# Performance work log

Measured on AMD Instinct MI355X. Metric: run time of the kernel, lower is better.

## Reference

```python
import jax, jax.numpy as jnp
import numpy as np

EPS = 0.0  # module eps default
N, C = 524288, 128


def setup_inputs() -> dict:
    key = jax.random.key(0)
    x = jax.random.normal(key, (N, C), dtype=jnp.float32)
    return {"x": x}


def reference(x):
    n, c = x.shape
    # mean over batch (H=W=1 in the original NCHW view)
    m = jnp.mean(x, axis=0, keepdims=True)          # [1, C]
    xn = x - m                                      # [N, C]
    # covariance: T @ T.T / (N-1) with T = xn.T -> [C, C]
    f_cov = jnp.einsum('ni,nj->ij', xn, xn) / (n - 1)
    eye = jnp.eye(c, dtype=x.dtype)
    f_cov_shrinked = (1.0 - EPS) * f_cov + EPS * eye
    L = jnp.linalg.cholesky(f_cov_shrinked)         # lower-triangular
    # inv_sqrt = L^{-1} via triangular solve of L @ X = I
    inv_sqrt = jax.scipy.linalg.solve_triangular(L, eye, lower=True)  # [C, C]
    # 1x1 conv with kernel inv_sqrt[o, i] == xn @ inv_sqrt.T
    decorrelated = xn @ inv_sqrt.T                  # [N, C]
    return decorrelated
```

## Files before the change

### kernel.cpp

```cpp
#include <hip/hip_runtime.h>

#define NROWS 524288
#define NCH 128
#define GSTR 40

typedef __attribute__((ext_vector_type(8))) short bf16x8;
typedef __attribute__((ext_vector_type(4))) float f32x4;

#define BARRIER_ND() asm volatile("s_waitcnt lgkmcnt(0)\ns_barrier" ::: "memory")

static __device__ __forceinline__ unsigned short f2bf_rne(float f) {
    unsigned u = __float_as_uint(f);
    return (unsigned short)((u + 0x7FFFu + ((u >> 16) & 1u)) >> 16);
}

static __device__ __forceinline__ bf16x8 ldfrag(const unsigned short* base, int c, int s0) {
    int m = (c >> 3) & 12;
    return *(const bf16x8*)(base + c * GSTR + 2 * (s0 ^ m));
}

#define PACKW1(B, c, x0, x1, csacc) do {                                      \
    unsigned u0 = __float_as_uint(x0), u1 = __float_as_uint(x1);              \
    unsigned packH = (u0 >> 16) | (u1 & 0xFFFF0000u);                         \
    float l0_ = 2.0f * ((x0) - __uint_as_float(u0 & 0xFFFF0000u));            \
    float l1_ = 2.0f * ((x1) - __uint_as_float(u1 & 0xFFFF0000u));            \
    unsigned packL = (unsigned)f2bf_rne(l0_) | ((unsigned)f2bf_rne(l1_) << 16); \
    int idx_ = (c) * GSTR + 2 * (p ^ (cg & 12));                              \
    *(unsigned*)&XT[B][0][idx_] = packH;                                      \
    *(unsigned*)&XT[B][1][idx_] = packL;                                      \
    csacc += (x0) + (x1);                                                     \
} while (0)

#define LOADR(ci, r0, r1, r2, r3) do {                                        \
    const float4* s4_ = (const float4*)x + ((size_t)(ci) * 32 + 2 * p) * 32 + cg * 2; \
    r0 = s4_[0]; r1 = s4_[1]; r2 = s4_[32]; r3 = s4_[33];                     \
} while (0)

#define PACKALL(B, r0, r1, r2, r3) do {                                       \
    PACKW1(B, cg * 8 + 0, r0.x, r2.x, cs0);                                   \
    PACKW1(B, cg * 8 + 1, r0.y, r2.y, cs1);                                   \
    PACKW1(B, cg * 8 + 2, r0.z, r2.z, cs2);                                   \
    PACKW1(B, cg * 8 + 3, r0.w, r2.w, cs3);                                   \
    PACKW1(B, cg * 8 + 4, r1.x, r3.x, cs4);                                   \
    PACKW1(B, cg * 8 + 5, r1.y, r3.y, cs5);                                   \
    PACKW1(B, cg * 8 + 6, r1.z, r3.z, cs6);                                   \
    PACKW1(B, cg * 8 + 7, r1.w, r3.w, cs7);                                   \
} while (0)

#define MFMA_STEP(B) do {                                                     \
    const unsigned short* Xh = &XT[B][0][0];                                  \
    const unsigned short* Xl = &XT[B][1][0];                                  \
    bf16x8 ah0 = ldfrag(Xh, (2 * w + 0) * 16 + lc, ls);                       \
    bf16x8 ah1 = ldfrag(Xh, (2 * w + 1) * 16 + lc, ls);                       \
    _Pragma("unroll")                                                         \
    for (int tj = 0; tj < 8; ++tj) {                                          \
        bf16x8 bh = ldfrag(Xh, tj * 16 + lc, ls);                             \
        bf16x8 bl = ldfrag(Xl, tj * 16 + lc, ls);                             \
        acc[0][tj] = __builtin_amdgcn_mfma_f32_16x16x32_bf16(ah0, bh, acc[0][tj], 0, 0, 0); \
        acc[0][tj] = __builtin_amdgcn_mfma_f32_16x16x32_bf16(ah0, bl, acc[0][tj], 0, 0, 0); \
        acc[1][tj] = __builtin_amdgcn_mfma_f32_16x16x32_bf16(ah1, bh, acc[1][tj], 0, 0, 0); \
        acc[1][tj] = __builtin_amdgcn_mfma_f32_16x16x32_bf16(ah1, bl, acc[1][tj], 0, 0, 0); \
    }                                                                         \
} while (0)

template <int STORE>
__global__ __launch_bounds__(256, 4) void k_gram(const float* __restrict__ x,
                                                 float* __restrict__ part,
                                                 float* __restrict__ colpart,
                                                 float* __restrict__ gram,
                                                 float* __restrict__ colsum,
                                                 int cpb) {
    __shared__ __align__(16) unsigned short XT[2][2][128 * GSTR];
    const int tid = threadIdx.x;
    const int w = tid >> 6;
    const int l = tid & 63;
    const int lc = l & 15;
    const int ls = (l >> 4) * 4;
    const int p = tid >> 4;
    const int cg = tid & 15;

    f32x4 acc[2][8];
#pragma unroll
    for (int a = 0; a < 2; ++a)
#pragma unroll
        for (int t = 0; t < 8; ++t) acc[a][t] = (f32x4){0.f, 0.f, 0.f, 0.f};
    float cs0 = 0.f, cs1 = 0.f, cs2 = 0.f, cs3 = 0.f;
    float cs4 = 0.f, cs5 = 0.f, cs6 = 0.f, cs7 = 0.f;

    const int c0 = blockIdx.x * cpb;
    float4 a0, a1, a2, a3, b0, b1, b2, b3;

    LOADR(c0 + 0, a0, a1, a2, a3);
    LOADR(c0 + 1, b0, b1, b2, b3);
    PACKALL(0, a0, a1, a2, a3);
    BARRIER_ND();

#pragma unroll 1
    for (int t = 0; t < cpb; t += 2) {
        MFMA_STEP(0);
        PACKALL(1, b0, b1, b2, b3);
        if (t + 2 < cpb) LOADR(c0 + t + 2, a0, a1, a2, a3);
        BARRIER_ND();
        MFMA_STEP(1);
        if (t + 2 < cpb) {
            PACKALL(0, a0, a1, a2, a3);
            if (t + 3 < cpb) LOADR(c0 + t + 3, b0, b1, b2, b3);
            BARRIER_ND();
        }
    }

    __syncthreads();
    float* cls = (float*)&XT[0][0][0];
    cls[(cg * 8 + 0) * 16 + p] = cs0;
    cls[(cg * 8 + 1) * 16 + p] = cs1;
    cls[(cg * 8 + 2) * 16 + p] = cs2;
    cls[(cg * 8 + 3) * 16 + p] = cs3;
    cls[(cg * 8 + 4) * 16 + p] = cs4;
    cls[(cg * 8 + 5) * 16 + p] = cs5;
    cls[(cg * 8 + 6) * 16 + p] = cs6;
    cls[(cg * 8 + 7) * 16 + p] = cs7;
    __syncthreads();
    float csr = 0.f;
    if (tid < 128) {
#pragma unroll
        for (int pp = 0; pp < 16; ++pp) csr += cls[tid * 16 + pp];
    }

    if (STORE) {
        float* pb = part + (size_t)blockIdx.x * 16384;
#pragma unroll
        for (int a = 0; a < 2; ++a)
#pragma unroll
            for (int tj = 0; tj < 8; ++tj)
#pragma unroll
                for (int q = 0; q < 4; ++q) {
                    int row = (2 * w + a) * 16 + (l >> 4) * 4 + q;
                    int col = tj * 16 + lc;
                    pb[row * NCH + col] = acc[a][tj][q];
                }
        if (tid < 128) colpart[blockIdx.x * 128 + tid] = csr;
    } else {
#pragma unroll
        for (int a = 0; a < 2; ++a)
#pragma unroll
            for (int tj = 0; tj < 8; ++tj)
#pragma unroll
                for (int q = 0; q < 4; ++q) {
                    int row = (2 * w + a) * 16 + (l >> 4) * 4 + q;
                    int col = tj * 16 + lc;
                    atomicAdd(&gram[row * NCH + col], acc[a][tj][q]);
                }
        if (tid < 128) atomicAdd(&colsum[tid], csr);
    }
}

__global__ __launch_bounds__(256) void k_reduce1(const float* __restrict__ part,
                                                 const float* __restrict__ colpart,
                                                 float* __restrict__ part2,
                                                 float* __restrict__ col2,
                                                 int NG) {
    const int b = blockIdx.x;
    if (b < 16 * NG) {
        const int g = b >> 4;
        const int sl = b & 15;
        const int e4 = sl * 1024 + threadIdx.x * 4;
        const float* p0 = part + (size_t)g * 32 * 16384 + e4;
        float4 s = {0.f, 0.f, 0.f, 0.f};
#pragma unroll
        for (int k = 0; k < 32; ++k) {
            float4 v = *(const float4*)(p0 + (size_t)k * 16384);
            s.x += v.x; s.y += v.y; s.z += v.z; s.w += v.w;
        }
        *(float4*)(part2 + (size_t)g * 16384 + e4) = s;
    } else {
        const int g = b - 16 * NG;
        if (threadIdx.x < 128) {
            const float* c0 = colpart + g * 32 * 128 + threadIdx.x;
            float s = 0.f;
#pragma unroll
            for (int k = 0; k < 32; ++k) s += c0[k * 128];
            col2[g * 128 + threadIdx.x] = s;
        }
    }
}

__global__ __launch_bounds__(256) void k_reduce2(const float* __restrict__ part2,
                                                 const float* __restrict__ col2,
                                                 float* __restrict__ gram,
                                                 float* __restrict__ colsum,
                                                 int NG) {
    const int b = blockIdx.x;
    if (b < 16) {
        const int e4 = b * 1024 + threadIdx.x * 4;
        float4 s = {0.f, 0.f, 0.f, 0.f};
#pragma unroll 8
        for (int g = 0; g < NG; ++g) {
            float4 v = *(const float4*)(part2 + (size_t)g * 16384 + e4);
            s.x += v.x; s.y += v.y; s.z += v.z; s.w += v.w;
        }
        *(float4*)(gram + e4) = s;
    } else if (threadIdx.x < 128) {
        float s = 0.f;
#pragma unroll 8
        for (int g = 0; g < NG; ++g) s += col2[g * 128 + threadIdx.x];
        colsum[threadIdx.x] = s;
    }
}

__global__ __launch_bounds__(1024) void k_chol(const float* __restrict__ gram,
                                               const float* __restrict__ colsum,
                                               float* __restrict__ Wout,
                                               float* __restrict__ mout) {
    __shared__ float C[128][264];
    __shared__ __align__(16) float Praw[2][4][264];
    __shared__ float m[128];
    __shared__ float dsq[128];
    const int tid = threadIdx.x;
    const int rs = tid >> 5;
    const int cs = tid & 31;

    if (tid < 128) {
        m[tid] = colsum[tid] * (1.0f / (float)NROWS);
        mout[tid] = m[tid];
    }
    __syncthreads();
    for (int idx = tid; idx < 128 * 128; idx += 1024) {
        int i = idx >> 7, j = idx & 127;
        float g = 0.5f * (gram[i * NCH + j] + gram[j * NCH + i]);
        C[i][128 + j] = (g - (float)NROWS * m[i] * m[j]) * (1.0f / (float)(NROWS - 1));
        C[i][j] = (i == j) ? 1.0f : 0.0f;
    }
    __syncthreads();
    if (tid < 264) {
        int r = tid / 66, g = tid % 66;
        *(float4*)&Praw[0][r][g * 4] = *(const float4*)&C[r][g * 4];
    }
    __syncthreads();

#pragma unroll 1
    for (int kb = 0; kb < 128; kb += 4) {
        const int buf = (kb >> 2) & 1;
        const float* P0 = Praw[buf][0];
        const float* P1 = Praw[buf][1];
        const float* P2 = Praw[buf][2];
        const float* P3 = Praw[buf][3];

        float M00 = P0[128 + kb + 0], M01 = P0[128 + kb + 1], M02 = P0[128 + kb + 2], M03 = P0[128 + kb + 3];
        float M10 = P1[128 + kb + 0], M11 = P1[128 + kb + 1], M12 = P1[128 + kb + 2], M13 = P1[128 + kb + 3];
        float M20 = P2[128 + kb + 0], M21 = P2[128 + kb + 1], M22 = P2[128 + kb + 2], M23 = P2[128 + kb + 3];
        float M30 = P3[128 + kb + 0], M31 = P3[128 + kb + 1], M32 = P3[128 + kb + 2], M33 = P3[128 + kb + 3];

        float rd0 = 1.0f / M00;
        float g10 = M10 * rd0, g20 = M20 * rd0, g30 = M30 * rd0;
        float N11 = M11 - g10 * M01, N12 = M12 - g10 * M02, N13 = M13 - g10 * M03;
        float N21 = M21 - g20 * M01, N22 = M22 - g20 * M02, N23 = M23 - g20 * M03;
        float N31 = M31 - g30 * M01, N32 = M32 - g30 * M02, N33 = M33 - g30 * M03;
        float rd1 = 1.0f / N11;
        float g21 = N21 * rd1, g31 = N31 * rd1;
        float P22 = N22 - g21 * N12, P23 = N23 - g21 * N13;
        float P32 = N32 - g31 * N12, P33 = N33 - g31 * N13;
        float rd2 = 1.0f / P22;
        float g32 = P32 * rd2;
        float Q33 = P33 - g32 * P23;
        float rd3 = 1.0f / Q33;

        float T10 = -g10;
        float T20 = -g20 - g21 * T10, T21 = -g21;
        float T30 = -g30 - g31 * T10 - g32 * T20;
        float T31 = -g31 - g32 * T21;
        float T32 = -g32;

        if (tid == 0) {
            dsq[kb + 0] = 1.0f / sqrtf(M00);
            dsq[kb + 1] = 1.0f / sqrtf(N11);
            dsq[kb + 2] = 1.0f / sqrtf(P22);
            dsq[kb + 3] = 1.0f / sqrtf(Q33);
        }

        const int gs = kb >> 2;
        const bool doB = (cs <= gs);
        const int gRel = gs + 1 + cs;
        const bool doA = (gRel < 32);

        float4 Pb0, Pb1, Pb2, Pb3, Pa0, Pa1, Pa2, Pa3;
        if (doB) {
            Pb0 = *(const float4*)&P0[cs * 4];
            Pb1 = *(const float4*)&P1[cs * 4];
            Pb2 = *(const float4*)&P2[cs * 4];
            Pb3 = *(const float4*)&P3[cs * 4];
        }
        if (doA) {
            Pa0 = *(const float4*)&P0[128 + gRel * 4];
            Pa1 = *(const float4*)&P1[128 + gRel * 4];
            Pa2 = *(const float4*)&P2[128 + gRel * 4];
            Pa3 = *(const float4*)&P3[128 + gRel * 4];
        }

        for (int j = kb + 1 + rs; j < 128; j += 32) {
            const int tmax = j - kb;
            float a0 = C[j][128 + kb + 0], a1 = C[j][128 + kb + 1];
            float a2 = C[j][128 + kb + 2], a3 = C[j][128 + kb + 3];
            float f0 = a0 * rd0;
            float c0 = f0, c1 = 0.f, c2 = 0.f, c3 = 0.f;
            if (tmax > 1) {
                float f1 = (a1 - c0 * M01) * rd1;
                c0 += f1 * T10; c1 = f1;
                if (tmax > 2) {
                    float f2 = (a2 - c0 * M02 - c1 * M12) * rd2;
                    c0 += f2 * T20; c1 += f2 * T21; c2 = f2;
                    if (tmax > 3) {
                        float f3 = (a3 - c0 * M03 - c1 * M13 - c2 * M23) * rd3;
                        c0 += f3 * T30; c1 += f3 * T31; c2 += f3 * T32; c3 = f3;
                    }
                }
            }
            const bool stage = (j >= kb + 4) && (j < kb + 8);
            if (doB) {
                float4 v = *(const float4*)&C[j][cs * 4];
                v.x -= c0 * Pb0.x + c1 * Pb1.x + c2 * Pb2.x + c3 * Pb3.x;
                v.y -= c0 * Pb0.y + c1 * Pb1.y + c2 * Pb2.y + c3 * Pb3.y;
                v.z -= c0 * Pb0.z + c1 * Pb1.z + c2 * Pb2.z + c3 * Pb3.z;
                v.w -= c0 * Pb0.w + c1 * Pb1.w + c2 * Pb2.w + c3 * Pb3.w;
                *(float4*)&C[j][cs * 4] = v;
                if (stage) *(float4*)&Praw[buf ^ 1][j - kb - 4][cs * 4] = v;
            }
            if (doA) {
                float4 v = *(const float4*)&C[j][128 + gRel * 4];
                v.x -= c0 * Pa0.x + c1 * Pa1.x + c2 * Pa2.x + c3 * Pa3.x;
                v.y -= c0 * Pa0.y + c1 * Pa1.y + c2 * Pa2.y + c3 * Pa3.y;
                v.z -= c0 * Pa0.z + c1 * Pa1.z + c2 * Pa2.z + c3 * Pa3.z;
                v.w -= c0 * Pa0.w + c1 * Pa1.w + c2 * Pa2.w + c3 * Pa3.w;
                *(float4*)&C[j][128 + gRel * 4] = v;
                if (stage) *(float4*)&Praw[buf ^ 1][j - kb - 4][128 + gRel * 4] = v;
            }
        }
        if (tid < 4 && kb + 4 < 128) {
            float4 e = {0.f, 0.f, 0.f, 0.f};
            ((float*)&e)[tid] = 1.0f;
            *(float4*)&Praw[buf ^ 1][tid][(gs + 1) * 4] = e;
        }
        __syncthreads();
    }

    for (int idx = tid; idx < 128 * 128; idx += 1024) {
        int j = idx >> 7, c = idx & 127;
        float vv = (c < j) ? C[j][c] * dsq[j] : ((c == j) ? dsq[j] : 0.0f);
        Wout[idx] = vv;
    }
}

__global__ __launch_bounds__(256, 3) void k_apply(const float* __restrict__ x,
                                                  const float* __restrict__ Wg,
                                                  const float* __restrict__ mg,
                                                  float* __restrict__ out) {
    __shared__ __align__(16) unsigned char XS[128 * 128];
    __shared__ float msh[128];
    const int tid = threadIdx.x;
    const int w = tid >> 6, l = tid & 63;
    const int lc = l & 15, la = l >> 4;

    if (tid < 32) *(float4*)&msh[tid * 4] = *(const float4*)&mg[tid * 4];
    __syncthreads();

    bf16x8 rfrag[2][4];
#pragma unroll
    for (int tjl = 0; tjl < 2; ++tjl) {
        int j = (w * 2 + tjl) * 16 + lc;
#pragma unroll
        for (int ks = 0; ks < 4; ++ks) {
            int i0 = ks * 32 + la * 8;
            float4 wa = *(const float4*)&Wg[j * 128 + i0];
            float4 wb = *(const float4*)&Wg[j * 128 + i0 + 4];
            rfrag[tjl][ks][0] = f2bf_rne(wa.x - ((j == i0 + 0) ? 1.0f : 0.0f));
            rfrag[tjl][ks][1] = f2bf_rne(wa.y - ((j == i0 + 1) ? 1.0f : 0.0f));
            rfrag[tjl][ks][2] = f2bf_rne(wa.z - ((j == i0 + 2) ? 1.0f : 0.0f));
            rfrag[tjl][ks][3] = f2bf_rne(wa.w - ((j == i0 + 3) ? 1.0f : 0.0f));
            rfrag[tjl][ks][4] = f2bf_rne(wb.x - ((j == i0 + 4) ? 1.0f : 0.0f));
            rfrag[tjl][ks][5] = f2bf_rne(wb.y - ((j == i0 + 5) ? 1.0f : 0.0f));
            rfrag[tjl][ks][6] = f2bf_rne(wb.z - ((j == i0 + 6) ? 1.0f : 0.0f));
            rfrag[tjl][ks][7] = f2bf_rne(wb.w - ((j == i0 + 7) ? 1.0f : 0.0f));
        }
    }

    f32x4 acc[8][2];
#pragma unroll
    for (int ti = 0; ti < 8; ++ti)
#pragma unroll
        for (int tjl = 0; tjl < 2; ++tjl) acc[ti][tjl] = (f32x4){0.f, 0.f, 0.f, 0.f};

    const size_t rowbase = (size_t)blockIdx.x * 128;

#pragma unroll
    for (int c = 0; c < 2; ++c) {
        const int kb = c * 64;
#pragma unroll
        for (int rep = 0; rep < 8; ++rep) {
            int f = tid + 256 * rep;
            int r = f >> 4, i4 = f & 15;
            float4 vx = *(const float4*)&x[(rowbase + r) * 128 + kb + i4 * 4];
            float4 mv = *(const float4*)&msh[kb + i4 * 4];
            unsigned b0 = f2bf_rne(vx.x - mv.x);
            unsigned b1 = f2bf_rne(vx.y - mv.y);
            unsigned b2 = f2bf_rne(vx.z - mv.z);
            unsigned b3 = f2bf_rne(vx.w - mv.w);
            unsigned off = r * 128 + ((((i4 >> 1) ^ (r & 7))) << 4) + (i4 & 1) * 8;
            *(uint2*)(XS + off) = make_uint2(b0 | (b1 << 16), b2 | (b3 << 16));
        }
        __syncthreads();
#pragma unroll
        for (int ksl = 0; ksl < 2; ++ksl) {
#pragma unroll
            for (int ti = 0; ti < 8; ++ti) {
                int r = ti * 16 + lc;
                int g = ksl * 4 + la;
                bf16x8 af = *(const bf16x8*)(XS + r * 128 + ((g ^ (r & 7)) << 4));
                acc[ti][0] = __builtin_amdgcn_mfma_f32_16x16x32_bf16(af, rfrag[0][c * 2 + ksl], acc[ti][0], 0, 0, 0);
                acc[ti][1] = __builtin_amdgcn_mfma_f32_16x16x32_bf16(af, rfrag[1][c * 2 + ksl], acc[ti][1], 0, 0, 0);
            }
        }
        __syncthreads();
    }

#pragma unroll
    for (int ti = 0; ti < 8; ++ti)
#pragma unroll
        for (int tjl = 0; tjl < 2; ++tjl)
#pragma unroll
            for (int q = 0; q < 4; ++q) {
                int rloc = ti * 16 + la * 4 + q;
                int cglob = (w * 2 + tjl) * 16 + lc;
                size_t a = (rowbase + rloc) * 128 + cglob;
                out[a] = (x[a] - msh[cglob]) + acc[ti][tjl][q];
            }
}

extern "C" void kernel_launch(void* const* d_in, const int* in_sizes, int n_in,
                              void* d_out, int out_size, void* d_ws, size_t ws_size,
                              hipStream_t stream) {
    const float* x = (const float*)d_in[0];
    float* ws = (float*)d_ws;
    float* gram = ws;
    float* colsum = ws + 16384;
    float* W = ws + 16512;
    float* m = ws + 32896;
    float* colpart = ws + 40960;
    float* part = ws + 172032;
    float* out = (float*)d_out;

    int nP = 0;
    for (int cand = 1024; cand >= 256; cand >>= 1) {
        int ng = cand / 32;
        size_t need = ((size_t)172032 + (size_t)cand * 16384 +
                       (size_t)ng * 16384 + (size_t)ng * 128) * sizeof(float);
        if (ws_size >= need) { nP = cand; break; }
    }

    if (nP > 0) {
        const int NG = nP / 32;
        float* part2 = part + (size_t)nP * 16384;
        float* col2 = part2 + (size_t)NG * 16384;
        int cpb = 16384 / nP;
        k_gram<1><<<nP, 256, 0, stream>>>(x, part, colpart, gram, colsum, cpb);
        k_reduce1<<<16 * NG + NG, 256, 0, stream>>>(part, colpart, part2, col2, NG);
        k_reduce2<<<17, 256, 0, stream>>>(part2, col2, gram, colsum, NG);
    } else {
        hipMemsetAsync(d_ws, 0, (16384 + 128) * sizeof(float), stream);
        k_gram<0><<<512, 256, 0, stream>>>(x, part, colpart, gram, colsum, 32);
    }
    k_chol<<<1, 1024, 0, stream>>>(gram, colsum, W, m);
    k_apply<<<NROWS / 128, 256, 0, stream>>>(x, W, m, out);
}
```

Baseline: 296.7 us.

## Stage full row tile in LDS and drop the residual re-read of x

The apply kernel now loads the whole 128x128 tile of centered x into LDS at once, in a 32KB buffer with a 16-way XOR swizzle, instead of two 64-column halves. It uses the full W matrix rather than W minus identity, so the output comes straight from the accumulator without reading x a second time from global memory. This removes one full read of x and one barrier round per half. In exchange, LDS per block doubles, which may cut occupancy, and the diagonal term is now computed in bf16 instead of exact fp32, which loses precision.

```diff
diff --git a/kernel.cpp b/kernel.cpp
--- a/kernel.cpp
+++ b/kernel.cpp
@@ -353,7 +353,7 @@
                                                   const float* __restrict__ Wg,
                                                   const float* __restrict__ mg,
                                                   float* __restrict__ out) {
-    __shared__ __align__(16) unsigned char XS[128 * 128];
+    __shared__ __align__(16) unsigned char XS[128 * 256];
     __shared__ float msh[128];
     const int tid = threadIdx.x;
     const int w = tid >> 6, l = tid & 63;
@@ -362,7 +362,7 @@
     if (tid < 32) *(float4*)&msh[tid * 4] = *(const float4*)&mg[tid * 4];
     __syncthreads();
 
-    bf16x8 rfrag[2][4];
+    bf16x8 wfrag[2][4];
 #pragma unroll
     for (int tjl = 0; tjl < 2; ++tjl) {
         int j = (w * 2 + tjl) * 16 + lc;
@@ -371,14 +371,14 @@
             int i0 = ks * 32 + la * 8;
             float4 wa = *(const float4*)&Wg[j * 128 + i0];
             float4 wb = *(const float4*)&Wg[j * 128 + i0 + 4];
-            rfrag[tjl][ks][0] = f2bf_rne(wa.x - ((j == i0 + 0) ? 1.0f : 0.0f));
-            rfrag[tjl][ks][1] = f2bf_rne(wa.y - ((j == i0 + 1) ? 1.0f : 0.0f));
-            rfrag[tjl][ks][2] = f2bf_rne(wa.z - ((j == i0 + 2) ? 1.0f : 0.0f));
-            rfrag[tjl][ks][3] = f2bf_rne(wa.w - ((j == i0 + 3) ? 1.0f : 0.0f));
-            rfrag[tjl][ks][4] = f2bf_rne(wb.x - ((j == i0 + 4) ? 1.0f : 0.0f));
-            rfrag[tjl][ks][5] = f2bf_rne(wb.y - ((j == i0 + 5) ? 1.0f : 0.0f));
-            rfrag[tjl][ks][6] = f2bf_rne(wb.z - ((j == i0 + 6) ? 1.0f : 0.0f));
-            rfrag[tjl][ks][7] = f2bf_rne(wb.w - ((j == i0 + 7) ? 1.0f : 0.0f));
+            wfrag[tjl][ks][0] = f2bf_rne(wa.x);
+            wfrag[tjl][ks][1] = f2bf_rne(wa.y);
+            wfrag[tjl][ks][2] = f2bf_rne(wa.z);
+            wfrag[tjl][ks][3] = f2bf_rne(wa.w);
+            wfrag[tjl][ks][4] = f2bf_rne(wb.x);
+            wfrag[tjl][ks][5] = f2bf_rne(wb.y);
+            wfrag[tjl][ks][6] = f2bf_rne(wb.z);
+            wfrag[tjl][ks][7] = f2bf_rne(wb.w);
         }
     }
 
@@ -391,36 +391,34 @@
     const size_t rowbase = (size_t)blockIdx.x * 128;
 
 #pragma unroll
-    for (int c = 0; c < 2; ++c) {
-        const int kb = c * 64;
-#pragma unroll
-        for (int rep = 0; rep < 8; ++rep) {
-            int f = tid + 256 * rep;
-            int r = f >> 4, i4 = f & 15;
-            float4 vx = *(const float4*)&x[(rowbase + r) * 128 + kb + i4 * 4];
-            float4 mv = *(const float4*)&msh[kb + i4 * 4];
-            unsigned b0 = f2bf_rne(vx.x - mv.x);
-            unsigned b1 = f2bf_rne(vx.y - mv.y);
-            unsigned b2 = f2bf_rne(vx.z - mv.z);
-            unsigned b3 = f2bf_rne(vx.w - mv.w);
-            unsigned off = r * 128 + ((((i4 >> 1) ^ (r & 7))) << 4) + (i4 & 1) * 8;
-            *(uint2*)(XS + off) = make_uint2(b0 | (b1 << 16), b2 | (b3 << 16));
-        }
-        __syncthreads();
-#pragma unroll
-        for (int ksl = 0; ksl < 2; ++ksl) {
-#pragma unroll
-            for (int ti = 0; ti < 8; ++ti) {
-                int r = ti * 16 + lc;
-                int g = ksl * 4 + la;
-                bf16x8 af = *(const bf16x8*)(XS + r * 128 + ((g ^ (r & 7)) << 4));
-                acc[ti][0] = __builtin_amdgcn_mfma_f32_16x16x32_bf16(af, rfrag[0][c * 2 + ksl], acc[ti][0], 0, 0, 0);
-                acc[ti][1] = __builtin_amdgcn_mfma_f32_16x16x32_bf16(af, rfrag[1][c * 2 + ksl], acc[ti][1], 0, 0, 0);
-            }
-        }
-        __syncthreads();
-    }
-
+    for (int rep = 0; rep < 16; ++rep) {
+        int f = tid + 256 * rep;
+        int r = f >> 5, i4 = f & 31;
+        float4 vx = *(const float4*)&x[(rowbase + r) * 128 + i4 * 4];
+        float4 mv = *(const float4*)&msh[i4 * 4];
+        unsigned b0 = f2bf_rne(vx.x - mv.x);
+        unsigned b1 = f2bf_rne(vx.y - mv.y);
+        unsigned b2 = f2bf_rne(vx.z - mv.z);
+        unsigned b3 = f2bf_rne(vx.w - mv.w);
+        int g = i4 >> 1, half = i4 & 1;
+        unsigned off = r * 256 + ((g ^ (r & 15)) << 4) + half * 8;
+        *(uint2*)(XS + off) = make_uint2(b0 | (b1 << 16), b2 | (b3 << 16));
+    }
+    __syncthreads();
+
+#pragma unroll
+    for (int ks = 0; ks < 4; ++ks) {
+#pragma unroll
+        for (int ti = 0; ti < 8; ++ti) {
+            int r = ti * 16 + lc;
+            int g = ks * 4 + la;
+            bf16x8 af = *(const bf16x8*)(XS + r * 256 + (((g ^ (r & 15))) << 4));
+            acc[ti][0] = __builtin_amdgcn_mfma_f32_16x16x32_bf16(af, wfrag[0][ks], acc[ti][0], 0, 0, 0);
+            acc[ti][1] = __builtin_amdgcn_mfma_f32_16x16x32_bf16(af, wfrag[1][ks], acc[ti][1], 0, 0, 0);
+        }
+    }
+
+    float* dst = out + rowbase * 128;
 #pragma unroll
     for (int ti = 0; ti < 8; ++ti)
 #pragma unroll
@@ -429,8 +427,7 @@
             for (int q = 0; q < 4; ++q) {
                 int rloc = ti * 16 + la * 4 + q;
                 int cglob = (w * 2 + tjl) * 16 + lc;
-                size_t a = (rowbase + rloc) * 128 + cglob;
-                out[a] = (x[a] - msh[cglob]) + acc[ti][tjl][q];
+                dst[rloc * 128 + cglob] = acc[ti][tjl][q];
             }
 }
 
```

Result: faster. 280.1 us (-5.6%).
